# Kernel tuning notes

Measured on AMD Instinct MI355X. Metric: run time of the kernel, lower is better.

The kernel has to match this reference:

```python
import jax, jax.numpy as jnp
import numpy as np

N = 100000; NFEAT = 256; NHID = 128; NCLASS = 40; DEG = 16; E = N * DEG
L = 2; AH = 16; ALPHA = 0.2; LP_ALPHA = 0.5


def setup_inputs() -> dict:
    key = jax.random.key(0)
    ks = jax.random.split(key, 12)
    s = 0.05
    x = jax.random.normal(ks[0], (N, NFEAT), jnp.float32)
    row = jnp.repeat(jnp.arange(N), DEG)                       # each node has DEG out-edges
    col = jax.random.randint(ks[1], (E,), 0, N)
    edges = jnp.stack([row, col])                              # [2, E]
    degree = jax.random.uniform(ks[2], (N, 1), jnp.float32, 0.5, 1.5)
    label = jax.random.uniform(ks[3], (N, NCLASS), jnp.float32)
    return {
        "x": x, "edges": edges, "degree": degree, "iftrain": 0, "label": label,
        "lb_w": jax.random.normal(ks[4], (NHID, NFEAT)) * s,
        "lb_b": jnp.zeros((NHID,)),
        "L2F": jax.random.normal(ks[5], (NCLASS, NHID)) * s,
        "Ws": jax.random.normal(ks[6], (L, 2 * NHID, NHID)) * s,
        "w2m": jax.random.normal(ks[7], (L, AH, NHID)) * s,
        "b2m": jnp.zeros((L, AH)),
        "ab": jnp.zeros((L, 1, AH + 1)),
        "lf1w": jax.random.normal(ks[8], (L, AH, (AH + 1) * 3)) * s,
        "lf1b": jnp.zeros((L, AH)),
        "lf2w": jax.random.normal(ks[9], (L, 1, AH)) * s,
        "lf2b": jnp.zeros((L, 1)),
        "LPW": jnp.ones((L, N, 1)),
        "la2w": jax.random.normal(ks[10], (NCLASS, NHID)) * s,
        "la2b": jnp.zeros((NCLASS,)),
    }


def _seg(vals, row, n):
    return jax.ops.segment_sum(vals, row, num_segments=n)


def _layer(x, pre_label, aggr, row, col, degree, lpw, W, w2m, b2m, ab, lf1w, lf1b, lf2w, lf2b):
    n = x.shape[0]
    # final_h = aggr * spmm(adj, LP_W*h*deg) * deg + (1-aggr) * h
    h = jnp.concatenate([x, pre_label], axis=1) @ W            # [N, nhid]
    agg = _seg((lpw * h * degree)[col], row, n)
    h = aggr * agg * degree + (1.0 - aggr) * h
    rowcnt = _seg(jnp.ones((row.shape[0], 1), x.dtype), row, n)  # [N,1] edges per row

    def mini(feat):
        m = feat @ w2m.T + b2m                                 # [N, AH]
        avg = _seg(m[col], row, n) / rowcnt                    # mean neighbor feature
        dist = jnp.sqrt(jnp.sum((avg[row] - m[col]) ** 2, -1) + 1e-12)  # [E]
        d2 = (_seg(dist, row, n) / rowcnt[:, 0])[:, None]      # row-wise mean distance
        return jnp.concatenate([m, d2], axis=1)                # [N, AH+1]

    def factor(hs, hd, hdiff):
        f = jnp.tanh(jnp.concatenate([hs, hd, hdiff], 1) @ lf1w.T + lf1b)
        return jax.nn.sigmoid((f @ lf2w.T + lf2b)[:, 0])       # [E]

    m0 = mini(h)
    hs0, hd0 = m0[row], m0[col]
    hdiff = jnp.abs(hd0 - hs0)
    f0 = factor(hs0, hd0, hdiff)
    m1 = mini(x)
    f1 = factor(m1[row] + ab, m1[col] + ab, hdiff)             # note: reuses hdiff (as in torch code)
    f1hop = (_seg(f1, row, n) / rowcnt[:, 0])[:, None]         # mean-reduce spmm
    f2hop = (_seg(f0 * f1hop[col, 0], row, n) / rowcnt[:, 0])[:, None]
    return jax.nn.leaky_relu(h, ALPHA), f2hop


def reference(x, edges, degree, iftrain, label, lb_w, lb_b, L2F, Ws, w2m, b2m, ab,
              lf1w, lf1b, lf2w, lf2b, LPW, la2w, la2b):
    row, col = edges[0], edges[1]
    h = x @ lb_w.T + lb_b
    pre_label = label @ L2F
    aggr = jnp.asarray(LP_ALPHA, h.dtype)
    for l in range(L):
        h, aggr = _layer(h, pre_label, aggr, row, col, degree, LPW[l], Ws[l],
                         w2m[l], b2m[l], ab[l], lf1w[l], lf1b[l], lf2w[l], lf2b[l])
    return jax.nn.log_softmax(h @ la2w.T + la2b, axis=-1)
```

## Files before the change

### kernel.cpp

```cpp
#include <hip/hip_runtime.h>
#include <hip/hip_bf16.h>
#include <hip/hip_fp8.h>
#include <math.h>

#define NN 100000
#define NCLS 40
#define DEGC 16
#define NEDGE (NN*DEGC)
#define ALPHAC 0.2f
#define LPALPHA 0.5f

typedef short short8v __attribute__((ext_vector_type(8)));
typedef float f32x4 __attribute__((ext_vector_type(4)));

__device__ __forceinline__ short f2bf(float f) {
    unsigned u = __float_as_uint(f);
    u += 0x7fff + ((u >> 16) & 1);
    return (short)(u >> 16);
}
__device__ __forceinline__ float bf2f(ushort u) {
    return __uint_as_float(((unsigned)u) << 16);
}
__device__ __forceinline__ unsigned char f2e4m3(float f) {
    __hip_fp8_e4m3 e(f);
    return (unsigned char)e.__x;
}
__device__ __forceinline__ void e4m3x4(unsigned u, float* o) {
#pragma unroll
    for (int s = 0; s < 4; ++s) {
        __hip_fp8_e4m3 e;
        e.__x = (__hip_fp8_storage_t)((u >> (8 * s)) & 0xff);
        o[s] = (float)e;
    }
}

template <int NCH1, bool ABF, bool HASL, bool WRT8, bool HASM1>
__global__ __launch_bounds__(256) void gemm128_lds(
    const void* __restrict__ A1v, const ushort* __restrict__ B1t,
    const ushort* __restrict__ labB64, const ushort* __restrict__ B2t,
    const float* __restrict__ bias, const float* __restrict__ biasm1,
    int leakyA, ushort* __restrict__ C,
    unsigned char* __restrict__ T8, ushort* __restrict__ M1out)
{
    constexpr int K1 = NCH1 * 32;
    constexpr int NG = NCH1 / 4;
    constexpr int NCH = NCH1 + (HASL ? 2 : 0);
    constexpr int BROWS = HASM1 ? 144 : 128;
    constexpr int NSLOT = BROWS / 16;
    __shared__ __align__(16) ushort Bs1[BROWS * 128];
    __shared__ __align__(16) ushort Bs2[HASL ? 128 * 64 : 8];

    const int tid = threadIdx.x;
    const int l   = tid & 63;
    const int w   = tid >> 6;
    const int lr  = l & 15;
    const int lk8 = (l >> 4) << 3;
    const int n0  = blockIdx.x * 64 + w * 16;
    int r = n0 + lr; r = r < NN ? r : NN - 1;
    const int swz = (lr & 7) << 4;

    short8v afr[NCH];
    if (ABF) {
        const ushort* __restrict__ A = (const ushort*)A1v;
#pragma unroll
        for (int kc = 0; kc < NCH1; ++kc)
            afr[kc] = *(const short8v*)(A + (size_t)r * K1 + kc * 32 + lk8);
    } else {
        const float* __restrict__ A = (const float*)A1v;
#pragma unroll
        for (int g = 0; g < NCH1; g += 2) {
            const float* p0 = A + (size_t)r * K1 + g * 32 + lk8;
            const float* p1 = A + (size_t)r * K1 + (g + 1) * 32 + lk8;
            float4 a0 = *(const float4*)p0;
            float4 a1 = *(const float4*)(p0 + 4);
            float4 b0 = *(const float4*)p1;
            float4 b1 = *(const float4*)(p1 + 4);
            short8v va, vb;
            va[0] = f2bf(a0.x); va[1] = f2bf(a0.y); va[2] = f2bf(a0.z); va[3] = f2bf(a0.w);
            va[4] = f2bf(a1.x); va[5] = f2bf(a1.y); va[6] = f2bf(a1.z); va[7] = f2bf(a1.w);
            vb[0] = f2bf(b0.x); vb[1] = f2bf(b0.y); vb[2] = f2bf(b0.z); vb[3] = f2bf(b0.w);
            vb[4] = f2bf(b1.x); vb[5] = f2bf(b1.y); vb[6] = f2bf(b1.z); vb[7] = f2bf(b1.w);
            afr[g] = va;
            afr[g + 1] = vb;
        }
    }
    if (HASL) {
        afr[NCH1]     = *(const short8v*)(labB64 + (size_t)r * 64 + lk8);
        afr[NCH1 + 1] = *(const short8v*)(labB64 + (size_t)r * 64 + 32 + lk8);
    }
    if (ABF && leakyA) {
#pragma unroll
        for (int kc = 0; kc < NCH1; ++kc)
#pragma unroll
            for (int j = 0; j < 8; ++j) {
                float f = bf2f((ushort)afr[kc][j]);
                f = f > 0.f ? f : ALPHAC * f;
                afr[kc][j] = f2bf(f);
            }
    }

    if (HASL) {
#pragma unroll
        for (int s = 0; s < 4; ++s) {
            const int slot = tid + s * 256;
            const int row = slot >> 3, colq = slot & 7;
            uint4 v = *(const uint4*)(B2t + (size_t)row * 64 + colq * 8);
            *(uint4*)((char*)Bs2 + ((row * 128 + colq * 16) ^ ((row & 7) << 4))) = v;
        }
    }

    f32x4 acc[8];
#pragma unroll
    for (int ni = 0; ni < 8; ++ni) acc[ni] = (f32x4){0.f, 0.f, 0.f, 0.f};
    f32x4 accm1 = (f32x4){0.f, 0.f, 0.f, 0.f};

#pragma unroll
    for (int g = 0; g < NG; ++g) {
        if (g) __syncthreads();
#pragma unroll
        for (int s = 0; s < NSLOT; ++s) {
            const int slot = tid + s * 256;
            const int row = slot >> 4, colq = slot & 15;
            uint4 v = *(const uint4*)(B1t + (size_t)row * K1 + g * 128 + colq * 8);
            *(uint4*)((char*)Bs1 + ((row * 256 + colq * 16) ^ ((row & 7) << 4))) = v;
        }
        __syncthreads();
#pragma unroll
        for (int ni = 0; ni < 8; ++ni) {
#pragma unroll
            for (int kc = 0; kc < 4; ++kc) {
                short8v b = *(const short8v*)((const char*)Bs1 +
                    (((ni * 16 + lr) * 256 + kc * 64 + lk8 * 2) ^ swz));
                acc[ni] = __builtin_amdgcn_mfma_f32_16x16x32_bf16(afr[g * 4 + kc], b, acc[ni], 0, 0, 0);
            }
        }
        if (HASM1) {
#pragma unroll
            for (int kc = 0; kc < 4; ++kc) {
                short8v b = *(const short8v*)((const char*)Bs1 +
                    (((128 + lr) * 256 + kc * 64 + lk8 * 2) ^ swz));
                accm1 = __builtin_amdgcn_mfma_f32_16x16x32_bf16(afr[g * 4 + kc], b, accm1, 0, 0, 0);
            }
        }
    }
    if (HASL) {
#pragma unroll
        for (int ni = 0; ni < 8; ++ni) {
#pragma unroll
            for (int kc = 0; kc < 2; ++kc) {
                short8v b = *(const short8v*)((const char*)Bs2 +
                    (((ni * 16 + lr) * 128 + kc * 64 + lk8 * 2) ^ swz));
                acc[ni] = __builtin_amdgcn_mfma_f32_16x16x32_bf16(afr[NCH1 + kc], b, acc[ni], 0, 0, 0);
            }
        }
    }

    const int rsub = (l >> 4) << 2;
#pragma unroll
    for (int ni = 0; ni < 8; ++ni) {
        const int cc = ni * 16 + lr;
        const float bv = bias ? bias[cc] : 0.f;
#pragma unroll
        for (int rg = 0; rg < 4; ++rg) {
            const int rr = n0 + rsub + rg;
            if (rr < NN) {
                const float v = acc[ni][rg] + bv;
                C[(size_t)rr * 128 + cc] = (ushort)f2bf(v);
                if (WRT8) T8[(size_t)rr * 128 + cc] = f2e4m3(v);
            }
        }
    }
    if (HASM1) {
        const float bm = biasm1[lr];
#pragma unroll
        for (int rg = 0; rg < 4; ++rg) {
            const int rr = n0 + rsub + rg;
            if (rr < NN)
                M1out[(size_t)rr * 32 + 16 + lr] = (ushort)f2bf(accm1[rg] + bm);
        }
    }
}

__global__ __launch_bounds__(256) void agg_v5(
    const unsigned char* __restrict__ T8, const ushort* __restrict__ hlin,
    const int* __restrict__ col, const float* __restrict__ sd,
    const float* __restrict__ degree, const float* __restrict__ aggrv,
    const float aggrs, int do_leaky, ushort* __restrict__ hout)
{
    const int lane = threadIdx.x & 63;
    const int node = blockIdx.x * 4 + (threadIdx.x >> 6);
    const int q  = lane >> 4;
    const int cq = lane & 15;

    int cl = 0; float sl = 0.f;
    if (lane < 16) {
        cl = col[node * 16 + lane];
        sl = sd[cl];
    }

    float ax[8];
#pragma unroll
    for (int s = 0; s < 8; ++s) ax[s] = 0.f;

#pragma unroll
    for (int g = 0; g < 4; ++g) {
        const int nb = g * 4 + q;
        const int   c  = __shfl(cl, nb, 64);
        const float wv = __shfl(sl, nb, 64);
        const uint2 u = *(const uint2*)(T8 + (size_t)c * 128 + cq * 8);
        float d0[4], d1[4];
        e4m3x4(u.x, d0);
        e4m3x4(u.y, d1);
#pragma unroll
        for (int s2 = 0; s2 < 4; ++s2) {
            ax[s2]     += wv * d0[s2];
            ax[4 + s2] += wv * d1[s2];
        }
    }
#pragma unroll
    for (int s = 0; s < 8; ++s) {
        ax[s] += __shfl_xor(ax[s], 16, 64);
        ax[s] += __shfl_xor(ax[s], 32, 64);
    }

    const uint4 us = *(const uint4*)(hlin + (size_t)node * 128 + cq * 8);
    const unsigned uus[4] = {us.x, us.y, us.z, us.w};
    const float a = aggrv ? aggrv[node] : aggrs;
    const float d = degree[node];
    uint4 uo;
    unsigned* uop = &uo.x;
#pragma unroll
    for (int s = 0; s < 4; ++s) {
        float ox = a * ax[(s < 2 ? s * 2 : (s - 2) * 2 + 4)] * d;
        float oy = a * ax[(s < 2 ? s * 2 + 1 : (s - 2) * 2 + 5)] * d;
        ox += (1.f - a) * bf2f((ushort)(uus[s] & 0xffff));
        oy += (1.f - a) * bf2f((ushort)(uus[s] >> 16));
        if (do_leaky) {
            ox = ox > 0.f ? ox : ALPHAC * ox;
            oy = oy > 0.f ? oy : ALPHAC * oy;
        }
        uop[s] = (unsigned)(ushort)f2bf(ox) | ((unsigned)(ushort)f2bf(oy) << 16);
    }
    if (q == 0)
        *(uint4*)(hout + (size_t)node * 128 + cq * 8) = uo;
}

__global__ __launch_bounds__(256) void gemm16_mfma(
    const ushort* __restrict__ A, const ushort* __restrict__ Wb,
    const float* __restrict__ bias, ushort* __restrict__ Mout, int ooff)
{
    __shared__ __align__(16) ushort Wl[16 * 128];
    const int tid = threadIdx.x;
    const int l  = tid & 63;
    const int w  = tid >> 6;
    const int lr = l & 15;
    const int lk = (l >> 4) << 3;
    const int swz = (lr & 7) << 4;
    {
        const int row = tid >> 4, colq = tid & 15;
        uint4 v = *(const uint4*)(Wb + (size_t)row * 128 + colq * 8);
        *(uint4*)((char*)Wl + ((row * 256 + colq * 16) ^ ((row & 7) << 4))) = v;
    }
    const int n0 = blockIdx.x * 64 + w * 16;
    int ar = n0 + lr; ar = ar < NN ? ar : NN - 1;
    short8v a[4];
#pragma unroll
    for (int kc = 0; kc < 4; ++kc)
        a[kc] = *(const short8v*)(A + (size_t)ar * 128 + kc * 32 + lk);
    __syncthreads();
    f32x4 acc = (f32x4){0.f, 0.f, 0.f, 0.f};
#pragma unroll
    for (int kc = 0; kc < 4; ++kc) {
        short8v b = *(const short8v*)((const char*)Wl + ((lr * 256 + kc * 64 + lk * 2) ^ swz));
        acc = __builtin_amdgcn_mfma_f32_16x16x32_bf16(a[kc], b, acc, 0, 0, 0);
    }
    const float bv = bias[lr];
    const int rb = n0 + ((l >> 4) << 2);
#pragma unroll
    for (int r = 0; r < 4; ++r) {
        int rr = rb + r;
        if (rr < NN) Mout[(size_t)rr * 32 + ooff + lr] = (ushort)f2bf(acc[r] + bv);
    }
}

__global__ __launch_bounds__(256) void mini2_dual(
    const ushort* __restrict__ Mb01, const int* __restrict__ col,
    float* __restrict__ d2_0, float* __restrict__ d2_1)
{
    __shared__ float sm0[16][16][17];
    __shared__ float sm1[16][16][17];
    __shared__ float av0[16][16];
    __shared__ float av1[16][16];
    const int tid = threadIdx.x;
    const int g = tid >> 4, j = tid & 15;
    const int node = blockIdx.x * 16 + g;
    const int c = col[node * 16 + j];
    const ushort* __restrict__ rowp = Mb01 + (size_t)c * 32;
    const uint4 u0 = *(const uint4*)rowp;
    const uint4 u1 = *(const uint4*)(rowp + 8);
    const uint4 u2 = *(const uint4*)(rowp + 16);
    const uint4 u3 = *(const uint4*)(rowp + 24);
    const unsigned w0[8] = {u0.x, u0.y, u0.z, u0.w, u1.x, u1.y, u1.z, u1.w};
    const unsigned w1[8] = {u2.x, u2.y, u2.z, u2.w, u3.x, u3.y, u3.z, u3.w};
#pragma unroll
    for (int s = 0; s < 8; ++s) {
        sm0[g][j][s * 2]     = bf2f((ushort)(w0[s] & 0xffff));
        sm0[g][j][s * 2 + 1] = bf2f((ushort)(w0[s] >> 16));
        sm1[g][j][s * 2]     = bf2f((ushort)(w1[s] & 0xffff));
        sm1[g][j][s * 2 + 1] = bf2f((ushort)(w1[s] >> 16));
    }
    __syncthreads();
    float a0 = 0.f, a1 = 0.f;
#pragma unroll
    for (int nb = 0; nb < 16; ++nb) { a0 += sm0[g][nb][j]; a1 += sm1[g][nb][j]; }
    av0[g][j] = a0 * (1.f / 16.f);
    av1[g][j] = a1 * (1.f / 16.f);
    __syncthreads();
    float dd0 = 1e-12f, dd1 = 1e-12f;
#pragma unroll
    for (int d = 0; d < 16; ++d) {
        float t0 = av0[g][d] - sm0[g][j][d];
        float t1 = av1[g][d] - sm1[g][j][d];
        dd0 += t0 * t0;
        dd1 += t1 * t1;
    }
    float dist0 = sqrtf(dd0), dist1 = sqrtf(dd1);
#pragma unroll
    for (int off = 1; off < 16; off <<= 1) {
        dist0 += __shfl_xor(dist0, off, 64);
        dist1 += __shfl_xor(dist1, off, 64);
    }
    if (j == 0) {
        d2_0[node] = dist0 * (1.f / 16.f);
        d2_1[node] = dist1 * (1.f / 16.f);
    }
}

__global__ __launch_bounds__(256) void prep_pnode(
    const ushort* __restrict__ Mb01, const float* __restrict__ d2_0,
    const float* __restrict__ d2_1,
    const float* __restrict__ ab, const float* __restrict__ lf1w,
    const float* __restrict__ lf1b,
    float* __restrict__ P0s, float* __restrict__ P1s,
    unsigned char* __restrict__ PK8)
{
    const int idx = blockIdx.x * 256 + threadIdx.x;
    const int i = idx >> 4, k = idx & 15;
    float m0[17], m1a[17];
    const ushort* r0 = Mb01 + (size_t)i * 32;
    const ushort* r1 = r0 + 16;
#pragma unroll
    for (int d = 0; d < 16; ++d) {
        m0[d]  = bf2f(r0[d]);
        m1a[d] = bf2f(r1[d]) + ab[d];
    }
    m0[16]  = d2_0[i];
    m1a[16] = d2_1[i] + ab[16];
    const float* __restrict__ Wk = lf1w + k * 51;
    float p0s = lf1b[k], p1s = p0s, p0d = 0.f, p1d = 0.f;
#pragma unroll
    for (int d = 0; d < 17; ++d) {
        const float w0 = Wk[d], w1 = Wk[17 + d];
        p0s += m0[d]  * w0;  p0d += m0[d]  * w1;
        p1s += m1a[d] * w0;  p1d += m1a[d] * w1;
    }
    P0s[idx] = p0s;
    P1s[idx] = p1s;
    unsigned char* __restrict__ pk = PK8 + (size_t)i * 64;
    pk[k]      = f2e4m3(m0[k]);
    pk[16 + k] = f2e4m3(p0d);
    pk[32 + k] = f2e4m3(p1d);
    if (k == 0) *(float*)(pk + 48) = d2_0[i];
}

__global__ __launch_bounds__(256) void fact2_kernel(
    const unsigned char* __restrict__ PK8,
    const float* __restrict__ P0s, const float* __restrict__ P1s,
    const int* __restrict__ col,
    const float* __restrict__ W2c, const float* __restrict__ lf2w,
    const float* __restrict__ lf2b,
    float* __restrict__ f0out, float* __restrict__ f1hout)
{
    const int e = blockIdx.x * 256 + threadIdx.x;
    const int i = e >> 4;
    const int c = col[e];

    const unsigned char* __restrict__ pki = PK8 + (size_t)i * 64;
    const unsigned char* __restrict__ pkc = PK8 + (size_t)c * 64;
    const uint4 mi8 = *(const uint4*)pki;
    const float d2i = *(const float*)(pki + 48);
    const uint4 mc8 = *(const uint4*)pkc;
    const uint4 p08 = *(const uint4*)(pkc + 16);
    const uint4 p18 = *(const uint4*)(pkc + 32);
    const float d2c = *(const float*)(pkc + 48);

    float mi[16], mc[16], P0d[16], P1d[16];
    e4m3x4(mi8.x, mi);     e4m3x4(mi8.y, mi + 4);
    e4m3x4(mi8.z, mi + 8); e4m3x4(mi8.w, mi + 12);
    e4m3x4(mc8.x, mc);     e4m3x4(mc8.y, mc + 4);
    e4m3x4(mc8.z, mc + 8); e4m3x4(mc8.w, mc + 12);
    e4m3x4(p08.x, P0d);     e4m3x4(p08.y, P0d + 4);
    e4m3x4(p08.z, P0d + 8); e4m3x4(p08.w, P0d + 12);
    e4m3x4(p18.x, P1d);     e4m3x4(p18.y, P1d + 4);
    e4m3x4(p18.z, P1d + 8); e4m3x4(p18.w, P1d + 12);

    float2 H2[8];
#pragma unroll
    for (int k2 = 0; k2 < 8; ++k2) H2[k2] = make_float2(0.f, 0.f);
#pragma unroll
    for (int d = 0; d < 16; ++d) {
        const float hd = fabsf(mc[d] - mi[d]);
        const float2* __restrict__ wv = (const float2*)(W2c + d * 16);
#pragma unroll
        for (int k2 = 0; k2 < 8; ++k2) {
            H2[k2].x = fmaf(hd, wv[k2].x, H2[k2].x);
            H2[k2].y = fmaf(hd, wv[k2].y, H2[k2].y);
        }
    }
    {
        const float hdd = fabsf(d2c - d2i);
        const float2* __restrict__ wv = (const float2*)(W2c + 16 * 16);
#pragma unroll
        for (int k2 = 0; k2 < 8; ++k2) {
            H2[k2].x = fmaf(hdd, wv[k2].x, H2[k2].x);
            H2[k2].y = fmaf(hdd, wv[k2].y, H2[k2].y);
        }
    }
    const float* __restrict__ H = (const float*)H2;

    const float* __restrict__ p0 = P0s + (size_t)i * 16;
    const float* __restrict__ p1 = P1s + (size_t)i * 16;
    float a0 = lf2b[0], a1 = a0;
#pragma unroll
    for (int k = 0; k < 16; ++k) {
        const float t0 = p0[k] + P0d[k] + H[k];
        const float t1 = p1[k] + P1d[k] + H[k];
        const float lw = lf2w[k];
        a0 += (1.f - 2.f / (__expf(2.f * t0) + 1.f)) * lw;
        a1 += (1.f - 2.f / (__expf(2.f * t1) + 1.f)) * lw;
    }
    f0out[e] = 1.f / (1.f + __expf(-a0));
    float f1 = 1.f / (1.f + __expf(-a1));
#pragma unroll
    for (int off = 1; off < 16; off <<= 1) f1 += __shfl_xor(f1, off, 64);
    if ((threadIdx.x & 15) == 0) f1hout[i] = f1 * (1.f / 16.f);
}

__global__ void f2hop_kernel(const float* __restrict__ f0, const float* __restrict__ f1h,
                             const int* __restrict__ col, float* __restrict__ out)
{
    const int i = blockIdx.x * 256 + threadIdx.x;
    if (i >= NN) return;
    float s = 0.f;
#pragma unroll
    for (int t = 0; t < 16; ++t) {
        int e = i * 16 + t;
        s += f0[e] * f1h[col[e]];
    }
    out[i] = s * (1.f / 16.f);
}

__global__ __launch_bounds__(256) void logits_mfma(
    const ushort* __restrict__ X, const ushort* __restrict__ Wb48,
    const float* __restrict__ bias, float* __restrict__ out)
{
    __shared__ __align__(16) ushort Wl[48 * 128];
    const int tid = threadIdx.x;
    const int l  = tid & 63;
    const int w  = tid >> 6;
    const int lr = l & 15;
    const int lk = (l >> 4) << 3;
    const int swz = (lr & 7) << 4;
#pragma unroll
    for (int s = 0; s < 6; ++s) {
        const int slot = tid + s * 256;
        const int row = slot >> 4, colq = slot & 15;
        uint4 v = *(const uint4*)(Wb48 + (size_t)row * 128 + colq * 8);
        *(uint4*)((char*)Wl + ((row * 256 + colq * 16) ^ ((row & 7) << 4))) = v;
    }
    const int row_base = blockIdx.x * 128 + w * 32;
    short8v afr[2][4];
#pragma unroll
    for (int mi = 0; mi < 2; ++mi) {
        int r = row_base + mi * 16 + lr;
        r = r < NN ? r : NN - 1;
#pragma unroll
        for (int kc = 0; kc < 4; ++kc)
            afr[mi][kc] = *(const short8v*)(X + (size_t)r * 128 + kc * 32 + lk);
    }
    __syncthreads();
    f32x4 acc[2][3];
#pragma unroll
    for (int mi = 0; mi < 2; ++mi)
#pragma unroll
        for (int ni = 0; ni < 3; ++ni) acc[mi][ni] = (f32x4){0.f, 0.f, 0.f, 0.f};
#pragma unroll
    for (int ni = 0; ni < 3; ++ni) {
#pragma unroll
        for (int kc = 0; kc < 4; ++kc) {
            short8v b = *(const short8v*)((const char*)Wl +
                (((ni * 16 + lr) * 256 + kc * 64 + lk * 2) ^ swz));
#pragma unroll
            for (int mi = 0; mi < 2; ++mi)
                acc[mi][ni] = __builtin_amdgcn_mfma_f32_16x16x32_bf16(afr[mi][kc], b, acc[mi][ni], 0, 0, 0);
        }
    }

    const float b0 = bias[lr];
    const float b1 = bias[16 + lr];
    const float b2 = (lr < 8) ? bias[32 + lr] : 0.f;
    const int rsub = (l >> 4) << 2;
#pragma unroll
    for (int mi = 0; mi < 2; ++mi) {
#pragma unroll
        for (int reg = 0; reg < 4; ++reg) {
            const int row = row_base + mi * 16 + rsub + reg;
            const float z0 = acc[mi][0][reg] + b0;
            const float z1 = acc[mi][1][reg] + b1;
            const float z2 = (lr < 8) ? acc[mi][2][reg] + b2 : -1e30f;
            float m = fmaxf(fmaxf(z0, z1), z2);
#pragma unroll
            for (int off = 1; off < 16; off <<= 1) m = fmaxf(m, __shfl_xor(m, off, 64));
            float s = __expf(z0 - m) + __expf(z1 - m) + ((lr < 8) ? __expf(z2 - m) : 0.f);
#pragma unroll
            for (int off = 1; off < 16; off <<= 1) s += __shfl_xor(s, off, 64);
            const float lg = m + __logf(s);
            if (row < NN) {
                float* __restrict__ po = out + (size_t)row * NCLS;
                po[lr] = z0 - lg;
                po[16 + lr] = z1 - lg;
                if (lr < 8) po[32 + lr] = z2 - lg;
            }
        }
    }
}

__global__ void prep_misc(
    const float* __restrict__ lb_w, const float* __restrict__ lb_b,
    const float* __restrict__ Ws, ushort* __restrict__ Wt1,
    const float* __restrict__ L2F, ushort* __restrict__ W2t,
    const float* __restrict__ la2w, ushort* __restrict__ Wb48,
    const float* __restrict__ lf1w, float* __restrict__ W2c,
    const float* __restrict__ w2m, ushort* __restrict__ W2mB,
    const float* __restrict__ b2m,
    const float* __restrict__ LPW, const float* __restrict__ degree,
    float* __restrict__ sd2, ushort* __restrict__ B1x,
    float* __restrict__ bias1, float* __restrict__ bm1e)
{
    int b = blockIdx.x;
    const int tid = threadIdx.x;
    if (b < 128) {
        int i = b * 256 + tid;
        int ll = i >> 14, r = i & 16383;
        int m = r >> 7, k = r & 127;
        Wt1[i] = (ushort)f2bf(Ws[(size_t)ll * 32768 + k * 128 + m]);
        return;
    }
    b -= 128;
    if (b < 64) {
        int i = b * 256 + tid;
        int ll = i >> 13, r = i & 8191;
        int m = r >> 6, c = r & 63;
        float acc = 0.f;
        if (c < NCLS) {
            const float* Wl = Ws + (size_t)ll * 32768 + 128 * 128;
            for (int j = 0; j < 128; ++j) acc += L2F[c * 128 + j] * Wl[j * 128 + m];
        }
        W2t[i] = (ushort)f2bf(acc);
        return;
    }
    b -= 64;
    if (b < 24) {
        int i = b * 256 + tid;
        if (i < 48 * 128) {
            int c = i >> 7;
            Wb48[i] = (c < NCLS) ? (ushort)f2bf(la2w[i]) : (ushort)0;
        }
        return;
    }
    b -= 24;
    if (b < 2) {
        int t = b * 256 + tid;
        if (t < 272) {
            int d = t >> 4, k = t & 15;
            W2c[t] = lf1w[k * 51 + 34 + d];
        }
        return;
    }
    b -= 2;
    if (b < 8) {
        int i = b * 256 + tid;
        W2mB[i] = (ushort)f2bf(w2m[i]);
        return;
    }
    b -= 8;
    if (b < 391) {
        int i = b * 256 + tid;
        if (i < NN) sd2[i] = LPW[i] * degree[i];
        return;
    }
    b -= 391;
    if (b < 391) {
        int i = b * 256 + tid;
        if (i < NN) sd2[NN + i] = LPW[NN + i] * degree[i];
        return;
    }
    b -= 391;
    if (b < 128) {
        int i = b * 256 + tid;
        int m = i >> 8, k = i & 255;
        float acc = 0.f;
        for (int mp = 0; mp < 128; ++mp)
            acc += lb_w[mp * 256 + k] * Ws[mp * 128 + m];
        B1x[(size_t)m * 256 + k] = (ushort)f2bf(acc);
        return;
    }
    b -= 128;
    if (b < 16) {
        int i = b * 256 + tid;
        int j = i >> 8, k = i & 255;
        float acc = 0.f;
        for (int mp = 0; mp < 128; ++mp)
            acc += lb_w[mp * 256 + k] * w2m[j * 128 + mp];
        B1x[(size_t)(128 + j) * 256 + k] = (ushort)f2bf(acc);
        return;
    }
    b -= 16;
    {
        if (tid < 128) {
            float acc = 0.f;
            for (int mp = 0; mp < 128; ++mp) acc += lb_b[mp] * Ws[mp * 128 + tid];
            bias1[tid] = acc;
        } else if (tid < 144) {
            const int j = tid - 128;
            float acc = b2m[j];
            for (int mp = 0; mp < 128; ++mp) acc += lb_b[mp] * w2m[j * 128 + mp];
            bm1e[j] = acc;
        }
    }
}

__global__ void cvt_label64v(const float* __restrict__ label, ushort* __restrict__ labB64)
{
    const int idx = blockIdx.x * 256 + threadIdx.x;
    const int i = idx >> 4;
    const int c0 = (idx & 15) * 4;
    ushort o[4];
#pragma unroll
    for (int j = 0; j < 4; ++j) {
        const int c = c0 + j;
        o[j] = (c < NCLS) ? (ushort)f2bf(label[(size_t)i * NCLS + c]) : (ushort)0;
    }
    *(uint2*)(labB64 + (size_t)i * 64 + c0) = make_uint2(
        (unsigned)o[0] | ((unsigned)o[1] << 16),
        (unsigned)o[2] | ((unsigned)o[3] << 16));
}

extern "C" void kernel_launch(void* const* d_in, const int* in_sizes, int n_in,
                              void* d_out, int out_size, void* d_ws, size_t ws_size,
                              hipStream_t stream)
{
    const float* x      = (const float*)d_in[0];
    const int*   edges  = (const int*)d_in[1];
    const float* degree = (const float*)d_in[2];
    const float* label  = (const float*)d_in[4];
    const float* lb_w   = (const float*)d_in[5];
    const float* lb_b   = (const float*)d_in[6];
    const float* L2F    = (const float*)d_in[7];
    const float* Ws     = (const float*)d_in[8];
    const float* w2m    = (const float*)d_in[9];
    const float* b2m    = (const float*)d_in[10];
    const float* ab     = (const float*)d_in[11];
    const float* lf1w   = (const float*)d_in[12];
    const float* lf1b   = (const float*)d_in[13];
    const float* lf2w   = (const float*)d_in[14];
    const float* lf2b   = (const float*)d_in[15];
    const float* LPW    = (const float*)d_in[16];
    const float* la2w   = (const float*)d_in[17];
    const float* la2b   = (const float*)d_in[18];
    const int* colp = edges + NEDGE;

    float* ws = (float*)d_ws;
    size_t o = 0;
    float* d2_0B = ws + o; o += NN;
    float* d2_1B = ws + o; o += NN;
    float* P0sB  = ws + o; o += (size_t)NN * 16;
    float* P1sB  = ws + o; o += (size_t)NN * 16;
    float* f0B   = ws + o; o += NEDGE;
    float* f1hB  = ws + o; o += NN;
    float* aggrB = ws + o; o += NN;
    float* sd2B  = ws + o; o += 2 * NN;
    float* W2cB  = ws + o; o += 272;
    float* bias1B = ws + o; o += 128;
    float* bm1eB  = ws + o; o += 16;
    ushort* bufA = (ushort*)(ws + o); o += (size_t)NN * 128 / 2;
    ushort* bufL = (ushort*)(ws + o); o += (size_t)NN * 128 / 2;
    ushort* labB64 = (ushort*)(ws + o); o += (size_t)NN * 64 / 2;
    ushort* Mb01 = (ushort*)(ws + o); o += (size_t)NN * 32 / 2;
    unsigned char* PK8 = (unsigned char*)(ws + o); o += (size_t)NN * 64 / 4;
    ushort* B1x  = (ushort*)(ws + o); o += 144 * 256 / 2;
    ushort* Wt1  = (ushort*)(ws + o); o += 2 * 128 * 128 / 2;
    ushort* W2t  = (ushort*)(ws + o); o += 2 * 128 * 64 / 2;
    ushort* W2mB = (ushort*)(ws + o); o += 16 * 128 / 2;
    ushort* Wb48 = (ushort*)(ws + o); o += 48 * 128 / 2;
    unsigned char* T8 = (unsigned char*)(ws + o); o += (size_t)NN * 128 / 4;

    dim3 b256(256);
    prep_misc<<<1153, b256, 0, stream>>>(lb_w, lb_b, Ws, Wt1, L2F, W2t, la2w, Wb48,
                                         lf1w, W2cB, w2m, W2mB, b2m, LPW, degree,
                                         sd2B, B1x, bias1B, bm1eB);
    cvt_label64v<<<6250, b256, 0, stream>>>(label, labB64);

    gemm128_lds<8, false, true, true, true><<<1563, b256, 0, stream>>>(
        x, B1x, labB64, W2t, bias1B, bm1eB, 0, bufL, T8, Mb01);
    agg_v5<<<25000, b256, 0, stream>>>(T8, bufL, colp, sd2B, degree,
                                       nullptr, LPALPHA, 0, bufA);
    gemm16_mfma<<<1563, b256, 0, stream>>>(bufA, W2mB, b2m, Mb01, 0);
    mini2_dual<<<6250, b256, 0, stream>>>(Mb01, colp, d2_0B, d2_1B);
    prep_pnode<<<6250, b256, 0, stream>>>(Mb01, d2_0B, d2_1B, ab, lf1w, lf1b,
                                          P0sB, P1sB, PK8);
    fact2_kernel<<<6250, b256, 0, stream>>>(PK8, P0sB, P1sB, colp,
                                            W2cB, lf2w, lf2b, f0B, f1hB);
    f2hop_kernel<<<391, b256, 0, stream>>>(f0B, f1hB, colp, aggrB);

    gemm128_lds<4, true, true, true, false><<<1563, b256, 0, stream>>>(
        bufA, Wt1 + 16384, labB64, W2t + 8192, nullptr, nullptr, 1, bufL, T8, nullptr);
    agg_v5<<<25000, b256, 0, stream>>>(T8, bufL, colp, sd2B + NN, degree,
                                       aggrB, 0.f, 1, bufA);

    logits_mfma<<<782, b256, 0, stream>>>(bufA, Wb48, la2b, (float*)d_out);
}
```

Before: 310.5 us.

## Fuse layer-1 mini projection into layer-2 input GEMM and drop gemm16 kernel

```diff
diff --git a/kernel.cpp b/kernel.cpp
--- a/kernel.cpp
+++ b/kernel.cpp
@@ -88,16 +88,6 @@
         afr[NCH1]     = *(const short8v*)(labB64 + (size_t)r * 64 + lk8);
         afr[NCH1 + 1] = *(const short8v*)(labB64 + (size_t)r * 64 + 32 + lk8);
     }
-    if (ABF && leakyA) {
-#pragma unroll
-        for (int kc = 0; kc < NCH1; ++kc)
-#pragma unroll
-            for (int j = 0; j < 8; ++j) {
-                float f = bf2f((ushort)afr[kc][j]);
-                f = f > 0.f ? f : ALPHAC * f;
-                afr[kc][j] = f2bf(f);
-            }
-    }
 
     if (HASL) {
 #pragma unroll
@@ -125,6 +115,25 @@
             *(uint4*)((char*)Bs1 + ((row * 256 + colq * 16) ^ ((row & 7) << 4))) = v;
         }
         __syncthreads();
+        if (HASM1) {
+#pragma unroll
+            for (int kc = 0; kc < 4; ++kc) {
+                short8v b = *(const short8v*)((const char*)Bs1 +
+                    (((128 + lr) * 256 + kc * 64 + lk8 * 2) ^ swz));
+                accm1 = __builtin_amdgcn_mfma_f32_16x16x32_bf16(
+                    afr[g * 4 + kc], b, accm1, 0, 0, 0);
+            }
+        }
+        if (ABF && leakyA && g == 0) {
+#pragma unroll
+            for (int kc = 0; kc < NCH1; ++kc)
+#pragma unroll
+                for (int j = 0; j < 8; ++j) {
+                    float f = bf2f((ushort)afr[kc][j]);
+                    f = f > 0.f ? f : ALPHAC * f;
+                    afr[kc][j] = f2bf(f);
+                }
+        }
 #pragma unroll
         for (int ni = 0; ni < 8; ++ni) {
 #pragma unroll
@@ -132,14 +141,6 @@
                 short8v b = *(const short8v*)((const char*)Bs1 +
                     (((ni * 16 + lr) * 256 + kc * 64 + lk8 * 2) ^ swz));
                 acc[ni] = __builtin_amdgcn_mfma_f32_16x16x32_bf16(afr[g * 4 + kc], b, acc[ni], 0, 0, 0);
-            }
-        }
-        if (HASM1) {
-#pragma unroll
-            for (int kc = 0; kc < 4; ++kc) {
-                short8v b = *(const short8v*)((const char*)Bs1 +
-                    (((128 + lr) * 256 + kc * 64 + lk8 * 2) ^ swz));
-                accm1 = __builtin_amdgcn_mfma_f32_16x16x32_bf16(afr[g * 4 + kc], b, accm1, 0, 0, 0);
             }
         }
     }
@@ -176,7 +177,7 @@
         for (int rg = 0; rg < 4; ++rg) {
             const int rr = n0 + rsub + rg;
             if (rr < NN)
-                M1out[(size_t)rr * 32 + 16 + lr] = (ushort)f2bf(accm1[rg] + bm);
+                M1out[(size_t)rr * 32 + lr] = (ushort)f2bf(accm1[rg] + bm);
         }
     }
 }
@@ -243,44 +244,6 @@
     }
     if (q == 0)
         *(uint4*)(hout + (size_t)node * 128 + cq * 8) = uo;
-}
-
-__global__ __launch_bounds__(256) void gemm16_mfma(
-    const ushort* __restrict__ A, const ushort* __restrict__ Wb,
-    const float* __restrict__ bias, ushort* __restrict__ Mout, int ooff)
-{
-    __shared__ __align__(16) ushort Wl[16 * 128];
-    const int tid = threadIdx.x;
-    const int l  = tid & 63;
-    const int w  = tid >> 6;
-    const int lr = l & 15;
-    const int lk = (l >> 4) << 3;
-    const int swz = (lr & 7) << 4;
-    {
-        const int row = tid >> 4, colq = tid & 15;
-        uint4 v = *(const uint4*)(Wb + (size_t)row * 128 + colq * 8);
-        *(uint4*)((char*)Wl + ((row * 256 + colq * 16) ^ ((row & 7) << 4))) = v;
-    }
-    const int n0 = blockIdx.x * 64 + w * 16;
-    int ar = n0 + lr; ar = ar < NN ? ar : NN - 1;
-    short8v a[4];
-#pragma unroll
-    for (int kc = 0; kc < 4; ++kc)
-        a[kc] = *(const short8v*)(A + (size_t)ar * 128 + kc * 32 + lk);
-    __syncthreads();
-    f32x4 acc = (f32x4){0.f, 0.f, 0.f, 0.f};
-#pragma unroll
-    for (int kc = 0; kc < 4; ++kc) {
-        short8v b = *(const short8v*)((const char*)Wl + ((lr * 256 + kc * 64 + lk * 2) ^ swz));
-        acc = __builtin_amdgcn_mfma_f32_16x16x32_bf16(a[kc], b, acc, 0, 0, 0);
-    }
-    const float bv = bias[lr];
-    const int rb = n0 + ((l >> 4) << 2);
-#pragma unroll
-    for (int r = 0; r < 4; ++r) {
-        int rr = rb + r;
-        if (rr < NN) Mout[(size_t)rr * 32 + ooff + lr] = (ushort)f2bf(acc[r] + bv);
-    }
 }
 
 __global__ __launch_bounds__(256) void mini2_dual(
@@ -537,26 +500,30 @@
 
 __global__ void prep_misc(
     const float* __restrict__ lb_w, const float* __restrict__ lb_b,
-    const float* __restrict__ Ws, ushort* __restrict__ Wt1,
+    const float* __restrict__ Ws, ushort* __restrict__ WtL1,
     const float* __restrict__ L2F, ushort* __restrict__ W2t,
     const float* __restrict__ la2w, ushort* __restrict__ Wb48,
     const float* __restrict__ lf1w, float* __restrict__ W2c,
-    const float* __restrict__ w2m, ushort* __restrict__ W2mB,
-    const float* __restrict__ b2m,
+    const float* __restrict__ w2m, const float* __restrict__ b2m,
     const float* __restrict__ LPW, const float* __restrict__ degree,
     float* __restrict__ sd2, ushort* __restrict__ B1x,
     float* __restrict__ bias1, float* __restrict__ bm1e)
 {
     int b = blockIdx.x;
     const int tid = threadIdx.x;
-    if (b < 128) {
-        int i = b * 256 + tid;
-        int ll = i >> 14, r = i & 16383;
-        int m = r >> 7, k = r & 127;
-        Wt1[i] = (ushort)f2bf(Ws[(size_t)ll * 32768 + k * 128 + m]);
-        return;
-    }
-    b -= 128;
+    if (b < 64) {
+        int i = b * 256 + tid;
+        int m = i >> 7, k = i & 127;
+        WtL1[(size_t)m * 128 + k] = (ushort)f2bf(Ws[32768 + (size_t)k * 128 + m]);
+        return;
+    }
+    b -= 64;
+    if (b < 16) {
+        int i = b * 256 + tid;
+        WtL1[128 * 128 + i] = (ushort)f2bf(w2m[i]);
+        return;
+    }
+    b -= 16;
     if (b < 64) {
         int i = b * 256 + tid;
         int ll = i >> 13, r = i & 8191;
@@ -588,12 +555,6 @@
         return;
     }
     b -= 2;
-    if (b < 8) {
-        int i = b * 256 + tid;
-        W2mB[i] = (ushort)f2bf(w2m[i]);
-        return;
-    }
-    b -= 8;
     if (b < 391) {
         int i = b * 256 + tid;
         if (i < NN) sd2[i] = LPW[i] * degree[i];
@@ -699,23 +660,25 @@
     ushort* Mb01 = (ushort*)(ws + o); o += (size_t)NN * 32 / 2;
     unsigned char* PK8 = (unsigned char*)(ws + o); o += (size_t)NN * 64 / 4;
     ushort* B1x  = (ushort*)(ws + o); o += 144 * 256 / 2;
-    ushort* Wt1  = (ushort*)(ws + o); o += 2 * 128 * 128 / 2;
+    ushort* WtL1 = (ushort*)(ws + o); o += 144 * 128 / 2;
     ushort* W2t  = (ushort*)(ws + o); o += 2 * 128 * 64 / 2;
-    ushort* W2mB = (ushort*)(ws + o); o += 16 * 128 / 2;
     ushort* Wb48 = (ushort*)(ws + o); o += 48 * 128 / 2;
     unsigned char* T8 = (unsigned char*)(ws + o); o += (size_t)NN * 128 / 4;
 
     dim3 b256(256);
-    prep_misc<<<1153, b256, 0, stream>>>(lb_w, lb_b, Ws, Wt1, L2F, W2t, la2w, Wb48,
-                                         lf1w, W2cB, w2m, W2mB, b2m, LPW, degree,
+    prep_misc<<<1097, b256, 0, stream>>>(lb_w, lb_b, Ws, WtL1, L2F, W2t, la2w, Wb48,
+                                         lf1w, W2cB, w2m, b2m, LPW, degree,
                                          sd2B, B1x, bias1B, bm1eB);
     cvt_label64v<<<6250, b256, 0, stream>>>(label, labB64);
 
     gemm128_lds<8, false, true, true, true><<<1563, b256, 0, stream>>>(
-        x, B1x, labB64, W2t, bias1B, bm1eB, 0, bufL, T8, Mb01);
+        x, B1x, labB64, W2t, bias1B, bm1eB, 0, bufL, T8, Mb01 + 16);
     agg_v5<<<25000, b256, 0, stream>>>(T8, bufL, colp, sd2B, degree,
                                        nullptr, LPALPHA, 0, bufA);
-    gemm16_mfma<<<1563, b256, 0, stream>>>(bufA, W2mB, b2m, Mb01, 0);
+
+    gemm128_lds<4, true, true, true, true><<<1563, b256, 0, stream>>>(
+        bufA, WtL1, labB64, W2t + 8192, nullptr, b2m, 1, bufL, T8, Mb01);
+
     mini2_dual<<<6250, b256, 0, stream>>>(Mb01, colp, d2_0B, d2_1B);
     prep_pnode<<<6250, b256, 0, stream>>>(Mb01, d2_0B, d2_1B, ab, lf1w, lf1b,
                                           P0sB, P1sB, PK8);
@@ -723,8 +686,6 @@
                                             W2cB, lf2w, lf2b, f0B, f1hB);
     f2hop_kernel<<<391, b256, 0, stream>>>(f0B, f1hB, colp, aggrB);
 
-    gemm128_lds<4, true, true, true, false><<<1563, b256, 0, stream>>>(
-        bufA, Wt1 + 16384, labB64, W2t + 8192, nullptr, nullptr, 1, bufL, T8, nullptr);
     agg_v5<<<25000, b256, 0, stream>>>(T8, bufL, colp, sd2B + NN, degree,
                                        aggrB, 0.f, 1, bufA);
 
```

Result: faster. 303.2 us (-2.3%).
